# Kernel tuning notes

Hardware: AMD Instinct MI355X
Metric: run time of the kernel (lower is better)

## Reference

```python
import jax, jax.numpy as jnp
import numpy as np

N, C_IN, H, W = 32, 128, 56, 56
C_OUT, KH, KW = 256, 3, 3
STRIDE = (1, 1)
PAD = (1, 1)


def setup_inputs() -> dict:
    key = jax.random.key(0)
    k_x, k_w, k_b = jax.random.split(key, 3)
    x = jax.random.normal(k_x, (N, C_IN, H, W), dtype=jnp.float32)
    # kaiming_uniform-like scale for weight, uniform bias in [-1/sqrt(fan_in), 1/sqrt(fan_in)]
    fan_in = C_IN * KH * KW
    bound_w = float(np.sqrt(6.0 / ((1 + 5.0) * fan_in)))  # kaiming_uniform a=sqrt(5)
    weight = jax.random.uniform(k_w, (C_OUT, C_IN, KH, KW), dtype=jnp.float32,
                                minval=-bound_w, maxval=bound_w)
    bound_b = float(1.0 / np.sqrt(fan_in))
    bias = jax.random.uniform(k_b, (C_OUT,), dtype=jnp.float32,
                              minval=-bound_b, maxval=bound_b)
    return {"x": x, "weight": weight, "bias": bias}


def reference(x, weight, bias):
    # Faithful math of the im2col conv: zero padding (ph,pw)=(1,1), stride 1,
    # groups=1 -> identical to a standard cross-correlation conv2d + bias.
    out = jax.lax.conv_general_dilated(
        x, weight,
        window_strides=STRIDE,
        padding=[(PAD[0], PAD[0]), (PAD[1], PAD[1])],
        dimension_numbers=("NCHW", "OIHW", "NCHW"),
    )
    return out + bias[None, :, None, None]
```

## Files before the change

kernel.cpp:

```cpp
#include <hip/hip_runtime.h>


#define NB   32
#define CIN  128
#define HH   56
#define WWD  56
#define COUT 256
#define HWP  3136
#define KTOT 1152
#define MTOT 100352

typedef __bf16 bf16x8 __attribute__((ext_vector_type(8)));
typedef float  f32x4  __attribute__((ext_vector_type(4)));
typedef unsigned short u16;

__device__ __forceinline__ u16 f2b(float f) {
  unsigned u = __float_as_uint(f);
  u += 0x7fffu + ((u >> 16) & 1u);
  return (u16)(u >> 16);
}

__device__ __forceinline__ void load_lds16(const void* g, void* l) {
  __builtin_amdgcn_global_load_lds(
      (const __attribute__((address_space(1))) unsigned int*)g,
      (__attribute__((address_space(3))) unsigned int*)l, 16, 0, 0);
}

__global__ __launch_bounds__(256) void k_transpose_x(const float* __restrict__ x,
                                                     u16* __restrict__ xt) {
  __shared__ float tile[32][33];
  const int n  = blockIdx.z;
  const int p0 = blockIdx.x * 32;
  const int c0 = blockIdx.y * 32;
  const int tx = threadIdx.x;
  const int ty = threadIdx.y;
  const float* xp = x + (size_t)n * CIN * HWP;
#pragma unroll
  for (int j = 0; j < 4; ++j) {
    int c = c0 + ty + j * 8;
    tile[ty + j * 8][tx] = xp[(size_t)c * HWP + p0 + tx];
  }
  __syncthreads();
  u16* xo = xt + (size_t)n * HWP * CIN;
#pragma unroll
  for (int j = 0; j < 4; ++j) {
    int p = p0 + ty + j * 8;
    xo[(size_t)p * CIN + c0 + tx] = f2b(tile[tx][ty + j * 8]);
  }
}

__global__ __launch_bounds__(256) void k_transform_w(const float* __restrict__ w,
                                                     u16* __restrict__ Wt,
                                                     u16* __restrict__ zb) {
  int o = blockIdx.x * 256 + threadIdx.x;
  if (o < COUT * KTOT) {
    int co  = o / KTOT;
    int rem = o - co * KTOT;
    int kk  = rem >> 7;
    int ci  = rem & 127;
    int kh  = kk / 3;
    int kw  = kk - kh * 3;
    Wt[o] = f2b(w[(((size_t)co * CIN + ci) * 3 + kh) * 3 + kw]);
  }
  if (blockIdx.x == 0 && threadIdx.x < 128) zb[threadIdx.x] = 0;
}

__global__ __launch_bounds__(256, 3) void k_conv_gemm(
    const u16* __restrict__ xt, const u16* __restrict__ Wt,
    const u16* __restrict__ zb, const float* __restrict__ bias,
    float* __restrict__ out) {
  __shared__ u16 lW[128 * 32];
  __shared__ u16 lX[128 * 32];

  const int tid  = threadIdx.x;
  const int wave = tid >> 6;
  const int lane = tid & 63;
  const int m0   = blockIdx.x * 128;
  const int co0  = blockIdx.y * 128;

  const int wrow = (wave >> 1) * 64;
  const int wcol = (wave & 1) * 64;

  const int koff8 = (lane & 3) * 8;
  const int rsub  = lane >> 2;

  int soh[2], sow[2], sbase[2];
#pragma unroll
  for (int t = 0; t < 2; ++t) {
    int chunk = wave * 2 + t;
    int m = m0 + chunk * 16 + rsub;
    int n = m / HWP;
    int s = m - n * HWP;
    int oh = s / WWD;
    int ow = s - oh * WWD;
    soh[t] = oh; sow[t] = ow;
    sbase[t] = n * HWP + oh * WWD + ow;
  }

  f32x4 acc[4][4];
#pragma unroll
  for (int i = 0; i < 4; ++i)
#pragma unroll
    for (int j = 0; j < 4; ++j) acc[i][j] = (f32x4){0.f, 0.f, 0.f, 0.f};

  const int r = lane & 15;
  const int q = lane >> 4;

  for (int kt = 0; kt < 36; ++kt) {
    const int ksp = kt >> 2;
    const int kh  = ksp / 3;
    const int kw  = ksp - kh * 3;
    const int ci0 = (kt & 3) << 5;
    const int kg  = kt << 5;

    __syncthreads();
#pragma unroll
    for (int t = 0; t < 2; ++t) {
      int chunk = wave * 2 + t;
      const u16* g = Wt + (size_t)(co0 + chunk * 16 + rsub) * KTOT + kg + koff8;
      load_lds16(g, &lW[chunk * 512]);
    }
#pragma unroll
    for (int t = 0; t < 2; ++t) {
      int chunk = wave * 2 + t;
      int ih = soh[t] + kh - 1;
      int iw = sow[t] + kw - 1;
      bool valid = ((unsigned)ih < HH) && ((unsigned)iw < WWD);
      const u16* g = valid
          ? xt + (size_t)(sbase[t] + (kh - 1) * WWD + (kw - 1)) * CIN + ci0 + koff8
          : zb + koff8;
      load_lds16(g, &lX[chunk * 512]);
    }
    __syncthreads();

    bf16x8 a[4], b[4];
#pragma unroll
    for (int ti = 0; ti < 4; ++ti)
      a[ti] = *(const bf16x8*)(&lW[(wrow + ti * 16 + r) * 32 + q * 8]);
#pragma unroll
    for (int tj = 0; tj < 4; ++tj)
      b[tj] = *(const bf16x8*)(&lX[(wcol + tj * 16 + r) * 32 + q * 8]);
#pragma unroll
    for (int ti = 0; ti < 4; ++ti)
#pragma unroll
      for (int tj = 0; tj < 4; ++tj)
        acc[ti][tj] =
            __builtin_amdgcn_mfma_f32_16x16x32_bf16(a[ti], b[tj], acc[ti][tj], 0, 0, 0);
  }

#pragma unroll
  for (int tj = 0; tj < 4; ++tj) {
    int m = m0 + wcol + tj * 16 + r;
    int n = m / HWP;
    int s = m - n * HWP;
#pragma unroll
    for (int ti = 0; ti < 4; ++ti) {
      f32x4 v = acc[ti][tj];
#pragma unroll
      for (int e = 0; e < 4; ++e) {
        int co = co0 + wrow + ti * 16 + q * 4 + e;
        out[((size_t)n * COUT + co) * HWP + s] = v[e] + bias[co];
      }
    }
  }
}

extern "C" void kernel_launch(void* const* d_in, const int* in_sizes, int n_in,
                              void* d_out, int out_size, void* d_ws, size_t ws_size,
                              hipStream_t stream) {
  const float* x    = (const float*)d_in[0];
  const float* w    = (const float*)d_in[1];
  const float* bias = (const float*)d_in[2];
  float* out        = (float*)d_out;

  u16* xt = (u16*)d_ws;
  u16* Wt = xt + (size_t)NB * HWP * CIN;
  u16* zb = Wt + (size_t)COUT * KTOT;

  k_transpose_x<<<dim3(98, 4, 32), dim3(32, 8), 0, stream>>>(x, xt);
  k_transform_w<<<dim3(1152), dim3(256), 0, stream>>>(w, Wt, zb);
  k_conv_gemm<<<dim3(784, 2), dim3(256), 0, stream>>>(xt, Wt, zb, bias, out);
}
```

Measured before the change: 232.1 us.

## Double K-tile depth with XOR-swizzled LDS and vectorize input transpose

The conv GEMM now stages 64-wide K slices per iteration instead of 32, halving the barrier and loop count, and uses an XOR swizzle on LDS column offsets to avoid bank conflicts on the wider rows. Launch bounds are raised to 4 blocks per SM. The input transpose kernel moves to 64x64 tiles with float4 loads, bf16 conversion before the LDS store, and 16-byte output writes. The risk is that doubled LDS per block and a higher occupancy target may cause register spills or limit residency.

```diff
diff --git a/kernel.cpp b/kernel.cpp
--- a/kernel.cpp
+++ b/kernel.cpp
@@ -13,6 +13,8 @@
 typedef __bf16 bf16x8 __attribute__((ext_vector_type(8)));
 typedef float  f32x4  __attribute__((ext_vector_type(4)));
 typedef unsigned short u16;
+typedef u16 u16x4 __attribute__((ext_vector_type(4)));
+typedef u16 u16x8 __attribute__((ext_vector_type(8)));
 
 __device__ __forceinline__ u16 f2b(float f) {
   unsigned u = __float_as_uint(f);
@@ -28,24 +30,34 @@
 
 __global__ __launch_bounds__(256) void k_transpose_x(const float* __restrict__ x,
                                                      u16* __restrict__ xt) {
-  __shared__ float tile[32][33];
+  __shared__ u16 tile[64][68];
   const int n  = blockIdx.z;
-  const int p0 = blockIdx.x * 32;
-  const int c0 = blockIdx.y * 32;
-  const int tx = threadIdx.x;
-  const int ty = threadIdx.y;
-  const float* xp = x + (size_t)n * CIN * HWP;
+  const int p0 = blockIdx.x * 64;
+  const int c0 = blockIdx.y * 64;
+  const int t  = threadIdx.x;
+
+  const float* xp = x + (size_t)n * CIN * HWP + (size_t)c0 * HWP + p0;
+  const int pl = (t & 15) * 4;
+  const int cr = t >> 4;
 #pragma unroll
   for (int j = 0; j < 4; ++j) {
-    int c = c0 + ty + j * 8;
-    tile[ty + j * 8][tx] = xp[(size_t)c * HWP + p0 + tx];
+    int c = cr + j * 16;
+    f32x4 v = *(const f32x4*)&xp[(size_t)c * HWP + pl];
+    u16x4 h;
+    h[0] = f2b(v[0]); h[1] = f2b(v[1]); h[2] = f2b(v[2]); h[3] = f2b(v[3]);
+    *(u16x4*)&tile[c][pl] = h;
   }
   __syncthreads();
-  u16* xo = xt + (size_t)n * HWP * CIN;
+  u16* xo = xt + (size_t)n * HWP * CIN + (size_t)p0 * CIN + c0;
+  const int ch = (t & 7) * 8;
+  const int pr = t >> 3;
 #pragma unroll
-  for (int j = 0; j < 4; ++j) {
-    int p = p0 + ty + j * 8;
-    xo[(size_t)p * CIN + c0 + tx] = f2b(tile[tx][ty + j * 8]);
+  for (int j = 0; j < 2; ++j) {
+    int p = pr + j * 32;
+    u16x8 o;
+#pragma unroll
+    for (int i = 0; i < 8; ++i) o[i] = tile[ch + i][p];
+    *(u16x8*)&xo[(size_t)p * CIN + ch] = o;
   }
 }
 
@@ -65,12 +77,12 @@
   if (blockIdx.x == 0 && threadIdx.x < 128) zb[threadIdx.x] = 0;
 }
 
-__global__ __launch_bounds__(256, 3) void k_conv_gemm(
+__global__ __launch_bounds__(256, 4) void k_conv_gemm(
     const u16* __restrict__ xt, const u16* __restrict__ Wt,
     const u16* __restrict__ zb, const float* __restrict__ bias,
     float* __restrict__ out) {
-  __shared__ u16 lW[128 * 32];
-  __shared__ u16 lX[128 * 32];
+  __shared__ u16 lW[128 * 64];
+  __shared__ u16 lX[128 * 64];
 
   const int tid  = threadIdx.x;
   const int wave = tid >> 6;
@@ -81,20 +93,20 @@
   const int wrow = (wave >> 1) * 64;
   const int wcol = (wave & 1) * 64;
 
-  const int koff8 = (lane & 3) * 8;
-  const int rsub  = lane >> 2;
+  const int rsub = lane >> 3;
+  const int pso  = (((lane & 7) ^ rsub)) * 8;
 
-  int soh[2], sow[2], sbase[2];
+  int soh[4], sow[4], sbase[4];
 #pragma unroll
-  for (int t = 0; t < 2; ++t) {
-    int chunk = wave * 2 + t;
-    int m = m0 + chunk * 16 + rsub;
+  for (int c = 0; c < 4; ++c) {
+    int chunk = wave * 4 + c;
+    int m = m0 + chunk * 8 + rsub;
     int n = m / HWP;
     int s = m - n * HWP;
     int oh = s / WWD;
     int ow = s - oh * WWD;
-    soh[t] = oh; sow[t] = ow;
-    sbase[t] = n * HWP + oh * WWD + ow;
+    soh[c] = oh; sow[c] = ow;
+    sbase[c] = n * HWP + oh * WWD + ow;
   }
 
   f32x4 acc[4][4];
@@ -103,49 +115,53 @@
 #pragma unroll
     for (int j = 0; j < 4; ++j) acc[i][j] = (f32x4){0.f, 0.f, 0.f, 0.f};
 
-  const int r = lane & 15;
-  const int q = lane >> 4;
+  const int r  = lane & 15;
+  const int q  = lane >> 4;
+  const int r7 = r & 7;
 
-  for (int kt = 0; kt < 36; ++kt) {
-    const int ksp = kt >> 2;
+  for (int kt = 0; kt < 18; ++kt) {
+    const int ksp = kt >> 1;
     const int kh  = ksp / 3;
     const int kw  = ksp - kh * 3;
-    const int ci0 = (kt & 3) << 5;
-    const int kg  = kt << 5;
+    const int ci0 = (kt & 1) << 6;
+    const int kg  = kt << 6;
 
     __syncthreads();
 #pragma unroll
-    for (int t = 0; t < 2; ++t) {
-      int chunk = wave * 2 + t;
-      const u16* g = Wt + (size_t)(co0 + chunk * 16 + rsub) * KTOT + kg + koff8;
-      load_lds16(g, &lW[chunk * 512]);
+    for (int c = 0; c < 4; ++c) {
+      int rowW = wave * 32 + c * 8;
+      const u16* g = Wt + (size_t)(co0 + rowW + rsub) * KTOT + kg + pso;
+      load_lds16(g, &lW[rowW * 64]);
     }
 #pragma unroll
-    for (int t = 0; t < 2; ++t) {
-      int chunk = wave * 2 + t;
-      int ih = soh[t] + kh - 1;
-      int iw = sow[t] + kw - 1;
+    for (int c = 0; c < 4; ++c) {
+      int ih = soh[c] + kh - 1;
+      int iw = sow[c] + kw - 1;
       bool valid = ((unsigned)ih < HH) && ((unsigned)iw < WWD);
       const u16* g = valid
-          ? xt + (size_t)(sbase[t] + (kh - 1) * WWD + (kw - 1)) * CIN + ci0 + koff8
-          : zb + koff8;
-      load_lds16(g, &lX[chunk * 512]);
+          ? xt + (size_t)(sbase[c] + (kh - 1) * WWD + (kw - 1)) * CIN + ci0 + pso
+          : zb + pso;
+      load_lds16(g, &lX[(wave * 32 + c * 8) * 64]);
     }
     __syncthreads();
 
-    bf16x8 a[4], b[4];
 #pragma unroll
-    for (int ti = 0; ti < 4; ++ti)
-      a[ti] = *(const bf16x8*)(&lW[(wrow + ti * 16 + r) * 32 + q * 8]);
+    for (int kk = 0; kk < 2; ++kk) {
+      bf16x8 a[4], b[4];
+      const int sw = ((kk * 4 + q) ^ r7) * 8;
 #pragma unroll
-    for (int tj = 0; tj < 4; ++tj)
-      b[tj] = *(const bf16x8*)(&lX[(wcol + tj * 16 + r) * 32 + q * 8]);
-#pragma unroll
-    for (int ti = 0; ti < 4; ++ti)
+      for (int ti = 0; ti < 4; ++ti)
+        a[ti] = *(const bf16x8*)(&lW[(wrow + ti * 16 + r) * 64 + sw]);
 #pragma unroll
       for (int tj = 0; tj < 4; ++tj)
-        acc[ti][tj] =
-            __builtin_amdgcn_mfma_f32_16x16x32_bf16(a[ti], b[tj], acc[ti][tj], 0, 0, 0);
+        b[tj] = *(const bf16x8*)(&lX[(wcol + tj * 16 + r) * 64 + sw]);
+#pragma unroll
+      for (int ti = 0; ti < 4; ++ti)
+#pragma unroll
+        for (int tj = 0; tj < 4; ++tj)
+          acc[ti][tj] =
+              __builtin_amdgcn_mfma_f32_16x16x32_bf16(a[ti], b[tj], acc[ti][tj], 0, 0, 0);
+    }
   }
 
 #pragma unroll
@@ -177,7 +193,7 @@
   u16* Wt = xt + (size_t)NB * HWP * CIN;
   u16* zb = Wt + (size_t)COUT * KTOT;
 
-  k_transpose_x<<<dim3(98, 4, 32), dim3(32, 8), 0, stream>>>(x, xt);
   k_transform_w<<<dim3(1152), dim3(256), 0, stream>>>(w, Wt, zb);
+  k_transpose_x<<<dim3(49, 2, 32), dim3(256), 0, stream>>>(x, xt);
   k_conv_gemm<<<dim3(784, 2), dim3(256), 0, stream>>>(xt, Wt, zb, bias, out);
 }
```

After: 207.6 us. 10.6% less time.
